# Kernel optimization log

Hardware: AMD Instinct MI355X
Metric: run time of the kernel (lower is better)

The kernel has to match this reference:

```python
import jax, jax.numpy as jnp
import numpy as np

# Config (mirrors HymbaLayer init + env constants)
DIM = 1024; NH = 16; NKV = 4; D = 64          # head_dim = DIM // NH
NATTN = NH // 2; NSSM = NH // 2; KVREP = NATTN // NKV
S = 16          # _HYMBA_SSM_STATE
NMETA = 4       # _HYMBA_META_TOK
BASE = 10000.0  # rope_base
CHUNK = 64      # _HYMBA_SCAN_CHUNK
B, T = 2, 2048


def _rms_norm(x, eps=1e-6):
    return x * jax.lax.rsqrt(jnp.mean(x * x, -1, keepdims=True) + eps)


def _rotary_cs(t_len, d, base):
    inv = 1.0 / (base ** (jnp.arange(0, d, 2, dtype=jnp.float32) / d))  # (d/2,)
    f = jnp.arange(t_len, dtype=jnp.float32)[:, None] * inv[None, :]    # (T, d/2)
    return jnp.cos(f), jnp.sin(f)


def _apply_rot(x, cos, sin):
    # x: (B, H, T, D); rotate-half style rotary
    d2 = x.shape[-1] // 2
    x1, x2 = x[..., :d2], x[..., d2:]
    c, s = cos[None, None], sin[None, None]
    return jnp.concatenate([x1 * c - x2 * s, x1 * s + x2 * c], -1)


def _scan_chunks(log_a, u, chunk):
    # Exact chunk-parallel diagonal scan: h_t = exp(log_a_t)*h_{t-1} + u_t
    b, t, s = u.shape
    nc = t // chunk
    la = log_a.reshape(b, nc, chunk, s)
    uu = u.reshape(b, nc, chunk, s)
    log_p = jnp.clip(jnp.cumsum(la, axis=2), -30.0, 0.0)
    p = jnp.exp(log_p)
    h_local = p * jnp.cumsum(uu * jnp.exp(-log_p), axis=2)

    def step(h0, args):
        hl, pc = args                          # (B, chunk, S)
        hc = hl + pc * h0[:, None, :]
        return hc[:, -1], hc

    _, hs = jax.lax.scan(step, jnp.zeros((b, s), u.dtype),
                         (jnp.swapaxes(h_local, 0, 1), jnp.swapaxes(p, 0, 1)))
    return jnp.swapaxes(hs, 0, 1).reshape(b, t, s)


def _mamba_head(logA, Bw, Cw, dtw, dtb, Ow, x):
    # x: (B, T, D); selective SSM with diagonal A
    dt = jnp.minimum(jax.nn.softplus(x @ dtw.T + dtb), 1.0)   # (B,T,S)
    A = jnp.minimum(-jnp.exp(logA), 10.0)                      # (S,)
    log_a = jnp.clip(dt * A, -0.5, 0.0)
    Bx = (x @ Bw.T) * dt
    Cc = x @ Cw.T
    h = _scan_chunks(log_a, Bx, CHUNK)                         # (B,T,S)
    y = jnp.sum(Cc * h, -1, keepdims=True)
    return h @ Ow.T + y * x[..., :1]


def _forward(x, meta_tokens, c_q_w, c_k_w, c_v_w, q_gain, ssm_in_w, proj_w,
             attn_scale, ssm_scale, ssm_logA, ssm_Bw, ssm_Cw, ssm_dtw, ssm_dtb, ssm_Ow):
    b, t, c = x.shape
    x_ext = jnp.concatenate([jnp.broadcast_to(meta_tokens, (b, NMETA, c)), x], 1)
    t_ext = t + NMETA
    q = (x_ext @ c_q_w.T).reshape(b, t_ext, NH, D).transpose(0, 2, 1, 3)
    k = (x_ext @ c_k_w.T).reshape(b, t_ext, NKV, D).transpose(0, 2, 1, 3)
    v = (x_ext @ c_v_w.T).reshape(b, t_ext, NKV, D).transpose(0, 2, 1, 3)
    q = _rms_norm(q); k = _rms_norm(k)
    cos, sin = _rotary_cs(t_ext, D, BASE)
    q = _apply_rot(q, cos, sin); k = _apply_rot(k, cos, sin)
    # GQA attention over the first NATTN heads, causal over T_ext
    q_attn = q[:, :NATTN] * q_gain[None, :, None, None]
    k_exp = jnp.repeat(k, KVREP, axis=1)
    v_exp = jnp.repeat(v, KVREP, axis=1)
    scores = jnp.einsum('bhqd,bhkd->bhqk', q_attn, k_exp) / jnp.sqrt(jnp.float32(D))
    mask = jnp.tril(jnp.ones((t_ext, t_ext), bool))
    scores = jnp.where(mask[None, None], scores, -jnp.inf)
    attn = jax.nn.softmax(scores, axis=-1)
    ao = jnp.einsum('bhqk,bhkd->bhqd', attn, v_exp)
    ao = ao[:, :, NMETA:].transpose(0, 2, 1, 3).reshape(b, t, NATTN * D) * attn_scale
    # SSM branch on the original (un-prepended) tokens
    ssm_x = (x @ ssm_in_w.T).reshape(b, t, NSSM, D)
    ssm_out = jax.vmap(_mamba_head, in_axes=(0, 0, 0, 0, 0, 0, 2), out_axes=2)(
        ssm_logA, ssm_Bw, ssm_Cw, ssm_dtw, ssm_dtb, ssm_Ow, ssm_x)
    ssm_out = ssm_out.reshape(b, t, NSSM * D) * ssm_scale
    return jnp.concatenate([ao, ssm_out], -1) @ proj_w.T


def setup_inputs() -> dict:
    key = jax.random.key(0)
    ks = jax.random.split(key, 16)
    r = lambda k, sh, sc=0.02: jax.random.normal(k, sh, jnp.float32) * sc
    return {
        'x': jax.random.normal(ks[0], (B, T, DIM), jnp.float32),
        'meta_tokens': r(ks[1], (1, NMETA, DIM)),
        'c_q_w': r(ks[2], (DIM, DIM)),
        'c_k_w': r(ks[3], (NKV * D, DIM)),
        'c_v_w': r(ks[4], (NKV * D, DIM)),
        'q_gain': jnp.full((NATTN,), 1.0, jnp.float32),
        'ssm_in_w': r(ks[5], (NSSM * D, DIM)),
        'proj_w': r(ks[6], (DIM, DIM)),
        'attn_scale': jnp.ones((1,), jnp.float32),
        'ssm_scale': jnp.ones((1,), jnp.float32),
        'ssm_logA': jax.random.normal(ks[7], (NSSM, S), jnp.float32) * 0.5,
        'ssm_Bw': r(ks[8], (NSSM, S, D), 0.05),
        'ssm_Cw': r(ks[9], (NSSM, S, D), 0.05),
        'ssm_dtw': r(ks[10], (NSSM, S, D), 0.05),
        'ssm_dtb': jnp.full((NSSM, S), -4.0, jnp.float32),
        'ssm_Ow': r(ks[11], (NSSM, D, S), 0.05),
    }


def reference(x, meta_tokens, c_q_w, c_k_w, c_v_w, q_gain, ssm_in_w, proj_w,
              attn_scale, ssm_scale, ssm_logA, ssm_Bw, ssm_Cw, ssm_dtw, ssm_dtb, ssm_Ow):
    return _forward(x, meta_tokens, c_q_w, c_k_w, c_v_w, q_gain, ssm_in_w, proj_w,
                    attn_scale, ssm_scale, ssm_logA, ssm_Bw, ssm_Cw, ssm_dtw, ssm_dtb, ssm_Ow)
```

## Files before the change

kernel.cpp:

```cpp
#include <hip/hip_runtime.h>
#include <hip/hip_bf16.h>
#include <math.h>

typedef __hip_bfloat16 bf16;
typedef __attribute__((ext_vector_type(8))) short short8;
typedef __attribute__((ext_vector_type(4))) float f32x4;

static constexpr int kB = 2;
static constexpr int kT = 2048;
static constexpr int kDIM = 1024;
static constexpr int kNMETA = 4;
static constexpr int kTEXT = kT + kNMETA;
static constexpr int kMEXT = kB * kTEXT;
static constexpr int kMPAD = 4224;
static constexpr int kMX = kB * kT;
static constexpr int kQT = 33;
static constexpr int kTP = 2112;

static constexpr size_t oXE = 0;
static constexpr size_t oYB = 0;
static constexpr size_t oLU = 8650752;
static constexpr size_t oCC = oLU + (size_t)kMX * 128 * 8;
static constexpr size_t oHL = oCC + (size_t)kMX * 128 * 4;
static constexpr size_t oPB = oHL + (size_t)kMX * 128 * 2;
static constexpr size_t oCH = oPB + (size_t)kMX * 128 * 2;
static constexpr size_t oCP = oCH + 16384 * 4;
static constexpr size_t oH0 = oCP + 16384 * 4;
static constexpr size_t oSX = oLU + (size_t)kMX * 128 * 8 + (size_t)kMX * 128 * 12;
static constexpr size_t oQP = oSX + (size_t)kMX * 512 * 2;
static constexpr size_t oKP = oQP + (size_t)kB * 8 * kTP * 64 * 2;
static constexpr size_t oVT = oKP + (size_t)kB * 4 * kTP * 64 * 2;
static constexpr size_t oWP = oVT + (size_t)kB * 4 * 64 * kTP * 2;
static constexpr size_t oWQ = oWP + (size_t)1024 * 1024 * 2;
static constexpr size_t oAO = 100663296;
static constexpr size_t oAL = oAO + (size_t)2 * kB * 8 * kTP * 64 * 4;

#define GLD_LDS16(gp, lp)                                                          \
  __builtin_amdgcn_global_load_lds((const __attribute__((address_space(1))) void*)(gp), \
                                   (__attribute__((address_space(3))) void*)(lp), 16, 0, 0)

__device__ __forceinline__ uint4 pack8(float4 a, float4 b) {
  union { bf16 h[8]; uint4 v; } u;
  u.h[0] = __float2bfloat16(a.x); u.h[1] = __float2bfloat16(a.y);
  u.h[2] = __float2bfloat16(a.z); u.h[3] = __float2bfloat16(a.w);
  u.h[4] = __float2bfloat16(b.x); u.h[5] = __float2bfloat16(b.y);
  u.h[6] = __float2bfloat16(b.z); u.h[7] = __float2bfloat16(b.w);
  return u.v;
}

__global__ __launch_bounds__(256) void prep_all(const float* __restrict__ cq, const float* __restrict__ ck,
                                                const float* __restrict__ cv, const float* __restrict__ sw,
                                                const float* __restrict__ pw,
                                                const float* __restrict__ x, const float* __restrict__ meta,
                                                bf16* __restrict__ wqkvsx, bf16* __restrict__ wproj,
                                                bf16* __restrict__ xe,
                                                bf16* __restrict__ Qp, bf16* __restrict__ Kp,
                                                bf16* __restrict__ Vt) {
  int i = blockIdx.x * 256 + threadIdx.x;
  if (i < 327680) {
    int row = i >> 7, v = i & 127;
    const float* src; bf16* dst;
    if (row < 512)       { src = cq + (size_t)row * 1024;          dst = wqkvsx + (size_t)row * 1024; }
    else if (row < 768)  { src = ck + (size_t)(row - 512) * 1024;  dst = wqkvsx + (size_t)row * 1024; }
    else if (row < 1024) { src = cv + (size_t)(row - 768) * 1024;  dst = wqkvsx + (size_t)row * 1024; }
    else if (row < 1536) { src = sw + (size_t)(row - 1024) * 1024; dst = wqkvsx + (size_t)row * 1024; }
    else                 { src = pw + (size_t)(row - 1536) * 1024; dst = wproj + (size_t)(row - 1536) * 1024; }
    float4 a0 = ((const float4*)src)[v * 2], a1 = ((const float4*)src)[v * 2 + 1];
    ((uint4*)dst)[v] = pack8(a0, a1);
  } else if (i < 868352) {
    int j = i - 327680;
    int r = j >> 7, v = j & 127;
    uint4 val = {0u, 0u, 0u, 0u};
    if (r < kMEXT) {
      int b = r / kTEXT, te = r - b * kTEXT;
      const float* src = (te < kNMETA) ? (meta + (size_t)te * kDIM)
                                       : (x + ((size_t)b * kT + (te - kNMETA)) * kDIM);
      float4 a0 = ((const float4*)src)[v * 2];
      float4 a1 = ((const float4*)src)[v * 2 + 1];
      val = pack8(a0, a1);
    }
    ((uint4*)(xe + (size_t)r * kDIM))[v] = val;
  } else {
    int j = i - 868352;
    if (j < 30720) {
      int k = j & 31, te = (j >> 5) % 60, bh = j / (60 * 32);
      *(unsigned int*)(Qp + ((size_t)bh * kTP + 2052 + te) * 64 + k * 2) = 0u;
    } else if (j < 46080) {
      int jj = j - 30720;
      int k = jj & 31, te = (jj >> 5) % 60, bh = jj / (60 * 32);
      *(unsigned int*)(Kp + ((size_t)bh * kTP + 2052 + te) * 64 + k * 2) = 0u;
    } else if (j < 61440) {
      int jj = j - 46080;
      int k = jj % 30, rowd = jj / 30;
      *(unsigned int*)(Vt + (size_t)rowd * kTP + 2052 + k * 2) = 0u;
    }
  }
}

template <int MODE>
__global__ __launch_bounds__(256) void gemm_t(const bf16* __restrict__ A,
                                              const bf16* __restrict__ W,
                                              void* __restrict__ O0, void* __restrict__ O1,
                                              void* __restrict__ O2, void* __restrict__ O3,
                                              const float* __restrict__ q_gain) {
  __shared__ short As[128 * 32];
  __shared__ short Bs[64 * 32];
  const int tid = threadIdx.x;
  const int wave = tid >> 6, lane = tid & 63;
  const int quad = lane >> 4, l16 = lane & 15;
  const int bm = blockIdx.y * 128, bn = blockIdx.x * 64;
  const int srow = tid >> 2, scol = (tid & 3) * 8;
  const bf16* ag0 = A + (size_t)(bm + srow) * 1024 + scol;
  const bf16* ag1 = A + (size_t)(bm + 64 + srow) * 1024 + scol;
  const bf16* bg0 = W + (size_t)(bn + srow) * 1024 + scol;
  char* asb = (char*)As + wave * 1024;
  char* bsb = (char*)Bs + wave * 1024;
  f32x4 acc[2][4] = {};
  for (int k0 = 0; k0 < 1024; k0 += 32) {
    __syncthreads();
    GLD_LDS16(ag0, asb);
    GLD_LDS16(ag1, asb + 4096);
    GLD_LDS16(bg0, bsb);
    ag0 += 32; ag1 += 32; bg0 += 32;
    __syncthreads();
    short8 af[2], bfr[4];
#pragma unroll
    for (int mi = 0; mi < 2; ++mi)
      af[mi] = *(const short8*)((const char*)As + (size_t)(wave * 32 + mi * 16 + l16) * 64 + quad * 16);
#pragma unroll
    for (int ni = 0; ni < 4; ++ni)
      bfr[ni] = *(const short8*)((const char*)Bs + (size_t)(ni * 16 + l16) * 64 + quad * 16);
#pragma unroll
    for (int mi = 0; mi < 2; ++mi)
#pragma unroll
      for (int ni = 0; ni < 4; ++ni)
        acc[mi][ni] = __builtin_amdgcn_mfma_f32_16x16x32_bf16(af[mi], bfr[ni], acc[mi][ni], 0, 0, 0);
  }
  if constexpr (MODE == 2) {
#pragma unroll
    for (int mi = 0; mi < 2; ++mi)
#pragma unroll
      for (int ni = 0; ni < 4; ++ni) {
        int colg = bn + ni * 16 + l16;
#pragma unroll
        for (int r = 0; r < 4; ++r) {
          int row = bm + wave * 32 + mi * 16 + quad * 4 + r;
          ((float*)O0)[(size_t)row * 1024 + colg] = acc[mi][ni][r];
        }
      }
  } else {
    const int tile = blockIdx.x;
    if (tile < 16) {
      float gain = (tile < 8) ? q_gain[tile] * 0.125f : 1.f;
      float inv0 = exp2f(-13.287712379549449f * (float)l16 * (1.f / 32.f));
      float inv1 = exp2f(-13.287712379549449f * (float)(l16 + 16) * (1.f / 32.f));
#pragma unroll
      for (int mi = 0; mi < 2; ++mi) {
        int row0 = bm + wave * 32 + mi * 16 + quad * 4;
        if (row0 >= kMEXT) continue;
        int b = row0 >= kTEXT ? 1 : 0;
        int te0 = row0 - b * kTEXT;
        if (tile < 12) {
          float ss[4];
#pragma unroll
          for (int r = 0; r < 4; ++r) {
            float s = 0.f;
#pragma unroll
            for (int ni = 0; ni < 4; ++ni) s += acc[mi][ni][r] * acc[mi][ni][r];
#pragma unroll
            for (int off = 1; off < 16; off <<= 1) s += __shfl_xor(s, off, 64);
            ss[r] = s;
          }
          bf16* base = (tile < 8)
            ? (bf16*)O0 + (((size_t)(b * 8 + tile)) * kTP + te0) * 64 + l16
            : (bf16*)O1 + (((size_t)(b * 4 + tile - 8)) * kTP + te0) * 64 + l16;
#pragma unroll
          for (int r = 0; r < 4; ++r) {
            float rn = rsqrtf(ss[r] * (1.f / 64.f) + 1e-6f) * gain;
            float te = (float)(te0 + r);
            float a0 = te * inv0, a1 = te * inv1;
            float c0 = __cosf(a0), s0 = __sinf(a0);
            float c1 = __cosf(a1), s1 = __sinf(a1);
            float v0 = acc[mi][0][r] * rn, v1 = acc[mi][1][r] * rn;
            float v2 = acc[mi][2][r] * rn, v3 = acc[mi][3][r] * rn;
            bf16* dst = base + (size_t)r * 64;
            dst[0]  = __float2bfloat16(v0 * c0 - v2 * s0);
            dst[16] = __float2bfloat16(v1 * c1 - v3 * s1);
            dst[32] = __float2bfloat16(v0 * s0 + v2 * c0);
            dst[48] = __float2bfloat16(v1 * s1 + v3 * c1);
          }
        } else {
          int hv = tile - 12;
#pragma unroll
          for (int ni = 0; ni < 4; ++ni) {
            union { unsigned long long q; bf16 hh[4]; } pw;
#pragma unroll
            for (int r = 0; r < 4; ++r) pw.hh[r] = __float2bfloat16(acc[mi][ni][r]);
            *(unsigned long long*)((bf16*)O2 +
                (((size_t)(b * 4 + hv)) * 64 + ni * 16 + l16) * kTP + te0) = pw.q;
          }
        }
      }
    } else {
#pragma unroll
      for (int mi = 0; mi < 2; ++mi)
#pragma unroll
        for (int ni = 0; ni < 4; ++ni) {
          int colg = bn - 1024 + ni * 16 + l16;
#pragma unroll
          for (int r = 0; r < 4; ++r) {
            int row = bm + wave * 32 + mi * 16 + quad * 4 + r;
            if (row < kMEXT) {
              int bb = row >= kTEXT ? 1 : 0;
              int te = row - bb * kTEXT;
              if (te >= kNMETA)
                ((bf16*)O3)[((size_t)(bb * kT + te - kNMETA)) * 512 + colg] =
                    __float2bfloat16(acc[mi][ni][r]);
            }
          }
        }
    }
  }
}

__global__ __launch_bounds__(256) void attn_part(const bf16* __restrict__ Qp,
                                                 const bf16* __restrict__ Kp,
                                                 const bf16* __restrict__ Vt,
                                                 float* __restrict__ AO, float* __restrict__ AL) {
  __shared__ short Ks[64][72];
  __shared__ short Vs[64][72];
  __shared__ short Ps[4][16][72];
  const int part = blockIdx.x & 1;
  const int qt = (kQT - 1) - (blockIdx.x >> 1);
  const int h = blockIdx.y, b = blockIdx.z;
  const int kvh = h >> 1;
  const int tid = threadIdx.x, wave = tid >> 6, lane = tid & 63;
  const int quad = lane >> 4, l16 = lane & 15;
  const int hsplit = (qt + 2) >> 1;
  const int kt_begin = part == 0 ? 0 : hsplit;
  const int kt_end = part == 0 ? hsplit : qt + 1;

  short8 qf[2];
  {
    const bf16* qrow = Qp + (((size_t)(b * 8 + h)) * kTP + qt * 64 + wave * 16 + l16) * 64 + quad * 8;
    qf[0] = *(const short8*)(qrow);
    qf[1] = *(const short8*)(qrow + 32);
  }
  short8 ones;
#pragma unroll
  for (int i = 0; i < 8; ++i) ones[i] = (short)0x3F80;

  const bf16* kbase = Kp + ((size_t)(b * 4 + kvh)) * kTP * 64;
  const bf16* vbase = Vt + ((size_t)(b * 4 + kvh)) * 64 * kTP;

  const int r0row = tid >> 3, r0c8 = tid & 7;
  const int r1row = (256 + tid) >> 3, r1c8 = tid & 7;

  f32x4 O[4] = {};
  f32x4 lacc = {};
  const int q_abs = qt * 64 + wave * 16 + l16;

  uint4 kr0 = *(const uint4*)(kbase + (size_t)(kt_begin * 64 + r0row) * 64 + r0c8 * 8);
  uint4 kr1 = *(const uint4*)(kbase + (size_t)(kt_begin * 64 + r1row) * 64 + r1c8 * 8);
  uint4 vr0 = *(const uint4*)(vbase + (size_t)r0row * kTP + kt_begin * 64 + r0c8 * 8);
  uint4 vr1 = *(const uint4*)(vbase + (size_t)r1row * kTP + kt_begin * 64 + r1c8 * 8);

  for (int kt = kt_begin; kt < kt_end; ++kt) {
    __syncthreads();
    *(uint4*)&Ks[r0row][r0c8 * 8] = kr0;
    *(uint4*)&Ks[r1row][r1c8 * 8] = kr1;
    *(uint4*)&Vs[r0row][r0c8 * 8] = vr0;
    *(uint4*)&Vs[r1row][r1c8 * 8] = vr1;
    if (kt + 1 < kt_end) {
      int kn = (kt + 1) * 64;
      kr0 = *(const uint4*)(kbase + (size_t)(kn + r0row) * 64 + r0c8 * 8);
      kr1 = *(const uint4*)(kbase + (size_t)(kn + r1row) * 64 + r1c8 * 8);
      vr0 = *(const uint4*)(vbase + (size_t)r0row * kTP + kn + r0c8 * 8);
      vr1 = *(const uint4*)(vbase + (size_t)r1row * kTP + kn + r1c8 * 8);
    }
    __syncthreads();

    f32x4 st[4] = {};
#pragma unroll
    for (int nb = 0; nb < 4; ++nb) {
      short8 ak0 = *(const short8*)&Ks[nb * 16 + l16][quad * 8];
      st[nb] = __builtin_amdgcn_mfma_f32_16x16x32_bf16(ak0, qf[0], st[nb], 0, 0, 0);
      short8 ak1 = *(const short8*)&Ks[nb * 16 + l16][32 + quad * 8];
      st[nb] = __builtin_amdgcn_mfma_f32_16x16x32_bf16(ak1, qf[1], st[nb], 0, 0, 0);
    }
    if (kt == qt) {
      int key0 = kt * 64 + quad * 4;
#pragma unroll
      for (int nb = 0; nb < 4; ++nb)
#pragma unroll
        for (int rg = 0; rg < 4; ++rg)
          if (key0 + nb * 16 + rg > q_abs) st[nb][rg] = -1e30f;
    }
#pragma unroll
    for (int nb = 0; nb < 4; ++nb) {
      union { unsigned long long q; bf16 hh[4]; } pw;
#pragma unroll
      for (int rg = 0; rg < 4; ++rg) pw.hh[rg] = __float2bfloat16(__expf(st[nb][rg]));
      *(unsigned long long*)&Ps[wave][l16][nb * 16 + quad * 4] = pw.q;
    }
    short8 pf0 = *(const short8*)&Ps[wave][l16][quad * 8];
    short8 pf1 = *(const short8*)&Ps[wave][l16][32 + quad * 8];
    lacc = __builtin_amdgcn_mfma_f32_16x16x32_bf16(pf0, ones, lacc, 0, 0, 0);
    lacc = __builtin_amdgcn_mfma_f32_16x16x32_bf16(pf1, ones, lacc, 0, 0, 0);
#pragma unroll
    for (int db = 0; db < 4; ++db) {
      short8 bv0 = *(const short8*)&Vs[db * 16 + l16][quad * 8];
      O[db] = __builtin_amdgcn_mfma_f32_16x16x32_bf16(pf0, bv0, O[db], 0, 0, 0);
      short8 bv1 = *(const short8*)&Vs[db * 16 + l16][32 + quad * 8];
      O[db] = __builtin_amdgcn_mfma_f32_16x16x32_bf16(pf1, bv1, O[db], 0, 0, 0);
    }
  }
  size_t hb = (((size_t)part * 2 + b) * 8 + h);
  float* aoB = AO + hb * kTP * 64;
  float* alB = AL + hb * kTP;
#pragma unroll
  for (int rg = 0; rg < 4; ++rg) {
    int q = qt * 64 + wave * 16 + quad * 4 + rg;
    float* dst = aoB + (size_t)q * 64 + l16;
#pragma unroll
    for (int db = 0; db < 4; ++db) dst[db * 16] = O[db][rg];
    if (l16 == 0) alB[q] = lacc[rg];
  }
}

__global__ __launch_bounds__(256) void ssm_prep(const bf16* __restrict__ sx,
                                                const float* __restrict__ dtw, const float* __restrict__ dtb,
                                                const float* __restrict__ Bw, const float* __restrict__ Cw,
                                                const float* __restrict__ logA,
                                                float* __restrict__ LU, float* __restrict__ Cc) {
  __shared__ short Xs[64][72];
  __shared__ short Ws[48][72];
  const int bm = blockIdx.x * 64, h = blockIdx.y;
  const int tid = threadIdx.x, wave = tid >> 6, lane = tid & 63;
  const int quad = lane >> 4, l16 = lane & 15;
#pragma unroll
  for (int is = 0; is < 2; ++is) {
    int e = is * 256 + tid;
    int row = e >> 3, v = e & 7;
    uint4 val = *(const uint4*)(sx + ((size_t)(bm + row)) * 512 + h * 64 + v * 8);
    *(uint4*)&Xs[row][v * 8] = val;
  }
#pragma unroll
  for (int is = 0; is < 2; ++is) {
    int s = is * 256 + tid;
    if (s < 384) {
      int row = s >> 3, v = s & 7;
      const float* src = (row < 16) ? dtw + ((size_t)(h * 16 + row)) * 64
                       : (row < 32) ? Bw + ((size_t)(h * 16 + row - 16)) * 64
                                    : Cw + ((size_t)(h * 16 + row - 32)) * 64;
      float4 a0 = ((const float4*)src)[v * 2];
      float4 a1 = ((const float4*)src)[v * 2 + 1];
      *(uint4*)&Ws[row][v * 8] = pack8(a0, a1);
    }
  }
  __syncthreads();
  short8 af0 = *(const short8*)&Xs[wave * 16 + l16][quad * 8];
  short8 af1 = *(const short8*)&Xs[wave * 16 + l16][32 + quad * 8];
  f32x4 acc[3] = {};
#pragma unroll
  for (int nb = 0; nb < 3; ++nb) {
    short8 b0 = *(const short8*)&Ws[nb * 16 + l16][quad * 8];
    acc[nb] = __builtin_amdgcn_mfma_f32_16x16x32_bf16(af0, b0, acc[nb], 0, 0, 0);
    short8 b1 = *(const short8*)&Ws[nb * 16 + l16][32 + quad * 8];
    acc[nb] = __builtin_amdgcn_mfma_f32_16x16x32_bf16(af1, b1, acc[nb], 0, 0, 0);
  }
  float dtb_v = dtb[h * 16 + l16];
  float A_v = fminf(-expf(logA[h * 16 + l16]), 10.f);
#pragma unroll
  for (int rg = 0; rg < 4; ++rg) {
    int bt = bm + wave * 16 + quad * 4 + rg;
    size_t ix = (size_t)bt * 128 + h * 16 + l16;
    float raw = acc[0][rg] + dtb_v;
    float sp = fmaxf(raw, 0.f) + log1pf(expf(-fabsf(raw)));
    float dt = fminf(sp, 1.f);
    float lav = fminf(fmaxf(dt * A_v, -0.5f), 0.f);
    *(float2*)(LU + 2 * ix) = make_float2(lav, acc[1][rg] * dt);
    Cc[ix] = acc[2][rg];
  }
}

__global__ __launch_bounds__(256) void ssm_scan1(const float* __restrict__ LU,
                                                 bf16* __restrict__ hloc, bf16* __restrict__ Pb,
                                                 float* __restrict__ chHt, float* __restrict__ chPt) {
  int id = blockIdx.x * 256 + threadIdx.x;
  if (id >= 16384) return;
  int hs = id & 127, c = (id >> 7) & 63, b = id >> 13;
  float hv = 0.f, cum = 0.f;
  size_t base = ((size_t)b * kT) * 128 + hs;
  const float2* LU2 = (const float2*)LU;
  for (int i = 0; i < 32; ++i) {
    size_t ix = base + (size_t)(c * 32 + i) * 128;
    float2 lu = LU2[ix];
    cum += lu.x;
    hv = expf(lu.x) * hv + lu.y;
    hloc[ix] = __float2bfloat16(hv);
    Pb[ix] = __float2bfloat16(expf(fmaxf(cum, -30.f)));
  }
  int t = b * 8192 + hs * 64 + c;
  chHt[t] = hv;
  chPt[t] = expf(fmaxf(cum, -30.f));
}

__global__ __launch_bounds__(256) void ssm_scan2(const float* __restrict__ chHt,
                                                 const float* __restrict__ chPt,
                                                 float* __restrict__ h0) {
  int id = blockIdx.x * 256 + threadIdx.x;
  int c = id & 63;
  int chain = id >> 6;
  int b = chain >> 7, hs = chain & 127;
  int t = b * 8192 + hs * 64 + c;
  float H = chHt[t], P = chPt[t];
#pragma unroll
  for (int off = 1; off < 64; off <<= 1) {
    float Hp = __shfl_up(H, off, 64);
    float Pp = __shfl_up(P, off, 64);
    if (c >= off) { H = H + P * Hp; P = P * Pp; }
  }
  float Hex = __shfl_up(H, 1, 64);
  if (c == 0) Hex = 0.f;
  h0[b * 8192 + c * 128 + hs] = Hex;
}

__global__ __launch_bounds__(256) void combine_out(const float* __restrict__ AO,
                                                   const float* __restrict__ AL,
                                                   const float* __restrict__ attn_scale,
                                                   const bf16* __restrict__ hloc, const bf16* __restrict__ Pb,
                                                   const float* __restrict__ h0, const float* __restrict__ Cc,
                                                   const bf16* __restrict__ sx, const float* __restrict__ Ow,
                                                   const float* __restrict__ ssm_scale,
                                                   bf16* __restrict__ Y) {
  if (blockIdx.x < 528) {
    int id = blockIdx.x * 256 + threadIdx.x;
    int d16 = id & 3;
    int tmp = id >> 2;
    int q = tmp % kTP; tmp /= kTP;
    int h = tmp & 7, b = tmp >> 3;
    if (q < kNMETA || q >= kTEXT) return;
    size_t hb0 = ((size_t)b * 8 + h), hb1 = ((size_t)(2 + b) * 8 + h);
    float l = AL[hb0 * kTP + q] + AL[hb1 * kTP + q];
    float so = attn_scale[0] / fmaxf(l, 1e-30f);
    const float4* p0 = (const float4*)(AO + (hb0 * kTP + q) * 64 + d16 * 16);
    const float4* p1 = (const float4*)(AO + (hb1 * kTP + q) * 64 + d16 * 16);
    bf16* dst = Y + ((size_t)(b * kT + q - kNMETA)) * kDIM + h * 64 + d16 * 16;
#pragma unroll
    for (int i = 0; i < 4; ++i) {
      float4 a = p0[i], c = p1[i];
      dst[i * 4 + 0] = __float2bfloat16((a.x + c.x) * so);
      dst[i * 4 + 1] = __float2bfloat16((a.y + c.y) * so);
      dst[i * 4 + 2] = __float2bfloat16((a.z + c.z) * so);
      dst[i * 4 + 3] = __float2bfloat16((a.w + c.w) * so);
    }
  } else {
    int id = (blockIdx.x - 528) * 256 + threadIdx.x;
    int d4 = id & 3, h = (id >> 2) & 7, t = (id >> 5) & 2047, b = id >> 16;
    size_t ix0 = ((size_t)(b * kT + t)) * 128 + h * 16;
    int h0b = b * 8192 + (t >> 5) * 128 + h * 16;
    float hv[16], y = 0.f;
#pragma unroll
    for (int s = 0; s < 16; ++s) {
      float v = __bfloat162float(hloc[ix0 + s]) + __bfloat162float(Pb[ix0 + s]) * h0[h0b + s];
      hv[s] = v;
      y += Cc[ix0 + s] * v;
    }
    float x0 = __bfloat162float(sx[((size_t)(b * kT + t)) * 512 + h * 64]);
    float scl = ssm_scale[0];
    const float* ow = Ow + ((size_t)h * 64 + d4 * 16) * 16;
    bf16* dst = Y + ((size_t)(b * kT + t)) * kDIM + 512 + h * 64 + d4 * 16;
    float yx = y * x0;
#pragma unroll
    for (int d = 0; d < 16; ++d) {
      float acc = yx;
      const float* owr = ow + d * 16;
#pragma unroll
      for (int s = 0; s < 16; ++s) acc += hv[s] * owr[s];
      dst[d] = __float2bfloat16(acc * scl);
    }
  }
}

extern "C" void kernel_launch(void* const* d_in, const int* in_sizes, int n_in,
                              void* d_out, int out_size, void* d_ws, size_t ws_size,
                              hipStream_t stream) {
  (void)in_sizes; (void)n_in; (void)out_size; (void)ws_size;
  const float* x        = (const float*)d_in[0];
  const float* meta     = (const float*)d_in[1];
  const float* c_q_w    = (const float*)d_in[2];
  const float* c_k_w    = (const float*)d_in[3];
  const float* c_v_w    = (const float*)d_in[4];
  const float* q_gain   = (const float*)d_in[5];
  const float* ssm_in_w = (const float*)d_in[6];
  const float* proj_w   = (const float*)d_in[7];
  const float* attn_sc  = (const float*)d_in[8];
  const float* ssm_sc   = (const float*)d_in[9];
  const float* ssm_logA = (const float*)d_in[10];
  const float* ssm_Bw   = (const float*)d_in[11];
  const float* ssm_Cw   = (const float*)d_in[12];
  const float* ssm_dtw  = (const float*)d_in[13];
  const float* ssm_dtb  = (const float*)d_in[14];
  const float* ssm_Ow   = (const float*)d_in[15];

  char* w = (char*)d_ws;
  bf16*  XE = (bf16*)(w + oXE);
  bf16*  SX = (bf16*)(w + oSX);
  bf16*  YB = (bf16*)(w + oYB);
  bf16*  QP = (bf16*)(w + oQP);
  bf16*  KP = (bf16*)(w + oKP);
  bf16*  VT = (bf16*)(w + oVT);
  bf16*  WQ = (bf16*)(w + oWQ);
  bf16*  WP = (bf16*)(w + oWP);
  float* LU = (float*)(w + oLU);
  float* CC = (float*)(w + oCC);
  bf16*  HL = (bf16*)(w + oHL);
  bf16*  PB = (bf16*)(w + oPB);
  float* CH = (float*)(w + oCH);
  float* CP = (float*)(w + oCP);
  float* H0 = (float*)(w + oH0);
  float* AO = (float*)(w + oAO);
  float* AL = (float*)(w + oAL);

  prep_all<<<3632, 256, 0, stream>>>(c_q_w, c_k_w, c_v_w, ssm_in_w, proj_w,
                                     x, meta, WQ, WP, XE, QP, KP, VT);

  gemm_t<0><<<dim3(24, kMPAD / 128), 256, 0, stream>>>(XE, WQ, QP, KP, VT, SX, q_gain);

  attn_part<<<dim3(kQT * 2, 8, kB), 256, 0, stream>>>(QP, KP, VT, AO, AL);

  ssm_prep<<<dim3(kMX / 64, 8), 256, 0, stream>>>(SX, ssm_dtw, ssm_dtb, ssm_Bw, ssm_Cw,
                                                  ssm_logA, LU, CC);
  ssm_scan1<<<64, 256, 0, stream>>>(LU, HL, PB, CH, CP);
  ssm_scan2<<<64, 256, 0, stream>>>(CH, CP, H0);

  combine_out<<<1040, 256, 0, stream>>>(AO, AL, attn_sc, HL, PB, H0, CC, SX, ssm_Ow, ssm_sc, YB);

  gemm_t<2><<<dim3(16, kMX / 128), 256, 0, stream>>>(YB, WP, d_out, nullptr, nullptr, nullptr, nullptr);
}
```

Baseline: 215.7 us.

## Fuse SSM input projection into QKV GEMM epilogue and merge scan passes

The SSM dt/B/C projection moves into the epilogue of the QKV GEMM, which works on the SSM-input tile from registers and LDS. This removes the separate ssm_prep kernel and the bf16 SX intermediate; only x0 per head is kept for combine_out. The two scan kernels become one kernel that computes chunk totals, scans across chunks in a wave, and then rescans to write the final h directly, dropping the Pb and h0 buffers. In exchange the scan reads LU twice, the GEMM epilogue does more work and uses more shared memory, and the final h is now computed in a sequential rescan rather than from bf16 partials.

```diff
diff --git a/kernel.cpp b/kernel.cpp
--- a/kernel.cpp
+++ b/kernel.cpp
@@ -22,22 +22,24 @@
 static constexpr size_t oLU = 8650752;
 static constexpr size_t oCC = oLU + (size_t)kMX * 128 * 8;
 static constexpr size_t oHL = oCC + (size_t)kMX * 128 * 4;
-static constexpr size_t oPB = oHL + (size_t)kMX * 128 * 2;
-static constexpr size_t oCH = oPB + (size_t)kMX * 128 * 2;
-static constexpr size_t oCP = oCH + 16384 * 4;
-static constexpr size_t oH0 = oCP + 16384 * 4;
-static constexpr size_t oSX = oLU + (size_t)kMX * 128 * 8 + (size_t)kMX * 128 * 12;
-static constexpr size_t oQP = oSX + (size_t)kMX * 512 * 2;
+static constexpr size_t oX0 = oHL + (size_t)kMX * 128 * 2;
+static constexpr size_t oQP = oX0 + (size_t)kMX * 8 * 4;
 static constexpr size_t oKP = oQP + (size_t)kB * 8 * kTP * 64 * 2;
 static constexpr size_t oVT = oKP + (size_t)kB * 4 * kTP * 64 * 2;
 static constexpr size_t oWP = oVT + (size_t)kB * 4 * 64 * kTP * 2;
 static constexpr size_t oWQ = oWP + (size_t)1024 * 1024 * 2;
-static constexpr size_t oAO = 100663296;
+static constexpr size_t oAO = 134217728;
 static constexpr size_t oAL = oAO + (size_t)2 * kB * 8 * kTP * 64 * 4;
 
 #define GLD_LDS16(gp, lp)                                                          \
   __builtin_amdgcn_global_load_lds((const __attribute__((address_space(1))) void*)(gp), \
                                    (__attribute__((address_space(3))) void*)(lp), 16, 0, 0)
+
+__device__ __forceinline__ short bf2s(float f) {
+  union { bf16 h; short s; } u;
+  u.h = __float2bfloat16(f);
+  return u.s;
+}
 
 __device__ __forceinline__ uint4 pack8(float4 a, float4 b) {
   union { bf16 h[8]; uint4 v; } u;
@@ -101,10 +103,15 @@
 __global__ __launch_bounds__(256) void gemm_t(const bf16* __restrict__ A,
                                               const bf16* __restrict__ W,
                                               void* __restrict__ O0, void* __restrict__ O1,
-                                              void* __restrict__ O2, void* __restrict__ O3,
-                                              const float* __restrict__ q_gain) {
-  __shared__ short As[128 * 32];
-  __shared__ short Bs[64 * 32];
+                                              void* __restrict__ O2,
+                                              const float* __restrict__ q_gain,
+                                              const float* __restrict__ dtw, const float* __restrict__ dtb,
+                                              const float* __restrict__ Bw, const float* __restrict__ Cw,
+                                              const float* __restrict__ logA,
+                                              float* __restrict__ LU, float* __restrict__ CC,
+                                              float* __restrict__ X0) {
+  constexpr int SMEM_SZ = (MODE == 0) ? 25344 : 12288;
+  __shared__ char smem[SMEM_SZ];
   const int tid = threadIdx.x;
   const int wave = tid >> 6, lane = tid & 63;
   const int quad = lane >> 4, l16 = lane & 15;
@@ -113,8 +120,8 @@
   const bf16* ag0 = A + (size_t)(bm + srow) * 1024 + scol;
   const bf16* ag1 = A + (size_t)(bm + 64 + srow) * 1024 + scol;
   const bf16* bg0 = W + (size_t)(bn + srow) * 1024 + scol;
-  char* asb = (char*)As + wave * 1024;
-  char* bsb = (char*)Bs + wave * 1024;
+  char* asb = smem + wave * 1024;
+  char* bsb = smem + 8192 + wave * 1024;
   f32x4 acc[2][4] = {};
   for (int k0 = 0; k0 < 1024; k0 += 32) {
     __syncthreads();
@@ -126,10 +133,10 @@
     short8 af[2], bfr[4];
 #pragma unroll
     for (int mi = 0; mi < 2; ++mi)
-      af[mi] = *(const short8*)((const char*)As + (size_t)(wave * 32 + mi * 16 + l16) * 64 + quad * 16);
+      af[mi] = *(const short8*)(smem + (size_t)(wave * 32 + mi * 16 + l16) * 64 + quad * 16);
 #pragma unroll
     for (int ni = 0; ni < 4; ++ni)
-      bfr[ni] = *(const short8*)((const char*)Bs + (size_t)(ni * 16 + l16) * 64 + quad * 16);
+      bfr[ni] = *(const short8*)(smem + 8192 + (size_t)(ni * 16 + l16) * 64 + quad * 16);
 #pragma unroll
     for (int mi = 0; mi < 2; ++mi)
 #pragma unroll
@@ -202,22 +209,72 @@
         }
       }
     } else {
-#pragma unroll
-      for (int mi = 0; mi < 2; ++mi)
-#pragma unroll
-        for (int ni = 0; ni < 4; ++ni) {
-          int colg = bn - 1024 + ni * 16 + l16;
+      const int hd = tile - 16;
+      __syncthreads();
+      short (*Xl)[72] = (short(*)[72])smem;
+      short (*Wl)[72] = (short(*)[72])(smem + 18432);
+#pragma unroll
+      for (int mi = 0; mi < 2; ++mi) {
+        if (l16 == 0) {
 #pragma unroll
           for (int r = 0; r < 4; ++r) {
             int row = bm + wave * 32 + mi * 16 + quad * 4 + r;
             if (row < kMEXT) {
               int bb = row >= kTEXT ? 1 : 0;
               int te = row - bb * kTEXT;
-              if (te >= kNMETA)
-                ((bf16*)O3)[((size_t)(bb * kT + te - kNMETA)) * 512 + colg] =
-                    __float2bfloat16(acc[mi][ni][r]);
+              if (te >= kNMETA) X0[(size_t)(bb * kT + te - kNMETA) * 8 + hd] = acc[mi][0][r];
             }
           }
+        }
+      }
+#pragma unroll
+      for (int mi = 0; mi < 2; ++mi)
+#pragma unroll
+        for (int ni = 0; ni < 4; ++ni)
+#pragma unroll
+          for (int r = 0; r < 4; ++r)
+            Xl[wave * 32 + mi * 16 + quad * 4 + r][ni * 16 + l16] = bf2s(acc[mi][ni][r]);
+      for (int s2 = tid; s2 < 384; s2 += 256) {
+        int row = s2 >> 3, v = s2 & 7;
+        const float* src = (row < 16) ? dtw + ((size_t)(hd * 16 + row)) * 64
+                         : (row < 32) ? Bw + ((size_t)(hd * 16 + row - 16)) * 64
+                                      : Cw + ((size_t)(hd * 16 + row - 32)) * 64;
+        float4 a0 = ((const float4*)src)[v * 2];
+        float4 a1 = ((const float4*)src)[v * 2 + 1];
+        *(uint4*)&Wl[row][v * 8] = pack8(a0, a1);
+      }
+      __syncthreads();
+      f32x4 a3[2][3] = {};
+#pragma unroll
+      for (int mt = 0; mt < 2; ++mt) {
+        short8 xa0 = *(const short8*)&Xl[wave * 32 + mt * 16 + l16][quad * 8];
+        short8 xa1 = *(const short8*)&Xl[wave * 32 + mt * 16 + l16][32 + quad * 8];
+#pragma unroll
+        for (int nb = 0; nb < 3; ++nb) {
+          short8 wb0 = *(const short8*)&Wl[nb * 16 + l16][quad * 8];
+          a3[mt][nb] = __builtin_amdgcn_mfma_f32_16x16x32_bf16(xa0, wb0, a3[mt][nb], 0, 0, 0);
+          short8 wb1 = *(const short8*)&Wl[nb * 16 + l16][32 + quad * 8];
+          a3[mt][nb] = __builtin_amdgcn_mfma_f32_16x16x32_bf16(xa1, wb1, a3[mt][nb], 0, 0, 0);
+        }
+      }
+      float dtb_v = dtb[hd * 16 + l16];
+      float A_v = fminf(-expf(logA[hd * 16 + l16]), 10.f);
+#pragma unroll
+      for (int mt = 0; mt < 2; ++mt)
+#pragma unroll
+        for (int r = 0; r < 4; ++r) {
+          int row = bm + wave * 32 + mt * 16 + quad * 4 + r;
+          if (row >= kMEXT) continue;
+          int bb = row >= kTEXT ? 1 : 0;
+          int te = row - bb * kTEXT;
+          if (te < kNMETA) continue;
+          size_t ix = (size_t)(bb * kT + te - kNMETA) * 128 + hd * 16 + l16;
+          float raw = a3[mt][0][r] + dtb_v;
+          float sp = fmaxf(raw, 0.f) + log1pf(expf(-fabsf(raw)));
+          float dt = fminf(sp, 1.f);
+          float lav = fminf(fmaxf(dt * A_v, -0.5f), 0.f);
+          *(float2*)(LU + 2 * ix) = make_float2(lav, a3[mt][1][r] * dt);
+          CC[ix] = a3[mt][2][r];
         }
     }
   }
@@ -328,110 +385,49 @@
   }
 }
 
-__global__ __launch_bounds__(256) void ssm_prep(const bf16* __restrict__ sx,
-                                                const float* __restrict__ dtw, const float* __restrict__ dtb,
-                                                const float* __restrict__ Bw, const float* __restrict__ Cw,
-                                                const float* __restrict__ logA,
-                                                float* __restrict__ LU, float* __restrict__ Cc) {
-  __shared__ short Xs[64][72];
-  __shared__ short Ws[48][72];
-  const int bm = blockIdx.x * 64, h = blockIdx.y;
-  const int tid = threadIdx.x, wave = tid >> 6, lane = tid & 63;
-  const int quad = lane >> 4, l16 = lane & 15;
-#pragma unroll
-  for (int is = 0; is < 2; ++is) {
-    int e = is * 256 + tid;
-    int row = e >> 3, v = e & 7;
-    uint4 val = *(const uint4*)(sx + ((size_t)(bm + row)) * 512 + h * 64 + v * 8);
-    *(uint4*)&Xs[row][v * 8] = val;
-  }
-#pragma unroll
-  for (int is = 0; is < 2; ++is) {
-    int s = is * 256 + tid;
-    if (s < 384) {
-      int row = s >> 3, v = s & 7;
-      const float* src = (row < 16) ? dtw + ((size_t)(h * 16 + row)) * 64
-                       : (row < 32) ? Bw + ((size_t)(h * 16 + row - 16)) * 64
-                                    : Cw + ((size_t)(h * 16 + row - 32)) * 64;
-      float4 a0 = ((const float4*)src)[v * 2];
-      float4 a1 = ((const float4*)src)[v * 2 + 1];
-      *(uint4*)&Ws[row][v * 8] = pack8(a0, a1);
-    }
-  }
+__global__ __launch_bounds__(256) void ssm_scan(const float* __restrict__ LU, bf16* __restrict__ HL) {
+  __shared__ float sH[4][64], sP[4][64], sH0[4][64];
+  const int tid = threadIdx.x;
+  const int ch = tid & 3, c = tid >> 2;
+  const int chain = blockIdx.x * 4 + ch;
+  const int b = chain >> 7, hs = chain & 127;
+  const float2* LU2 = (const float2*)LU;
+  const size_t base = ((size_t)b * kT) * 128 + hs;
+  float H = 0.f, cum = 0.f;
+  for (int i = 0; i < 32; ++i) {
+    float2 lu = LU2[base + (size_t)(c * 32 + i) * 128];
+    cum += lu.x;
+    H = __expf(lu.x) * H + lu.y;
+  }
+  sH[ch][c] = H;
+  sP[ch][c] = __expf(cum);
   __syncthreads();
-  short8 af0 = *(const short8*)&Xs[wave * 16 + l16][quad * 8];
-  short8 af1 = *(const short8*)&Xs[wave * 16 + l16][32 + quad * 8];
-  f32x4 acc[3] = {};
-#pragma unroll
-  for (int nb = 0; nb < 3; ++nb) {
-    short8 b0 = *(const short8*)&Ws[nb * 16 + l16][quad * 8];
-    acc[nb] = __builtin_amdgcn_mfma_f32_16x16x32_bf16(af0, b0, acc[nb], 0, 0, 0);
-    short8 b1 = *(const short8*)&Ws[nb * 16 + l16][32 + quad * 8];
-    acc[nb] = __builtin_amdgcn_mfma_f32_16x16x32_bf16(af1, b1, acc[nb], 0, 0, 0);
-  }
-  float dtb_v = dtb[h * 16 + l16];
-  float A_v = fminf(-expf(logA[h * 16 + l16]), 10.f);
-#pragma unroll
-  for (int rg = 0; rg < 4; ++rg) {
-    int bt = bm + wave * 16 + quad * 4 + rg;
-    size_t ix = (size_t)bt * 128 + h * 16 + l16;
-    float raw = acc[0][rg] + dtb_v;
-    float sp = fmaxf(raw, 0.f) + log1pf(expf(-fabsf(raw)));
-    float dt = fminf(sp, 1.f);
-    float lav = fminf(fmaxf(dt * A_v, -0.5f), 0.f);
-    *(float2*)(LU + 2 * ix) = make_float2(lav, acc[1][rg] * dt);
-    Cc[ix] = acc[2][rg];
-  }
-}
-
-__global__ __launch_bounds__(256) void ssm_scan1(const float* __restrict__ LU,
-                                                 bf16* __restrict__ hloc, bf16* __restrict__ Pb,
-                                                 float* __restrict__ chHt, float* __restrict__ chPt) {
-  int id = blockIdx.x * 256 + threadIdx.x;
-  if (id >= 16384) return;
-  int hs = id & 127, c = (id >> 7) & 63, b = id >> 13;
-  float hv = 0.f, cum = 0.f;
-  size_t base = ((size_t)b * kT) * 128 + hs;
-  const float2* LU2 = (const float2*)LU;
+  const int wv = tid >> 6, lane = tid & 63;
+  float Hs = sH[wv][lane], Ps = sP[wv][lane];
+#pragma unroll
+  for (int off = 1; off < 64; off <<= 1) {
+    float Hp = __shfl_up(Hs, off, 64);
+    float Pp = __shfl_up(Ps, off, 64);
+    if (lane >= off) { Hs = Hs + Ps * Hp; Ps = Ps * Pp; }
+  }
+  float Hex = __shfl_up(Hs, 1, 64);
+  if (lane == 0) Hex = 0.f;
+  sH0[wv][lane] = Hex;
+  __syncthreads();
+  float h = sH0[ch][c];
   for (int i = 0; i < 32; ++i) {
     size_t ix = base + (size_t)(c * 32 + i) * 128;
     float2 lu = LU2[ix];
-    cum += lu.x;
-    hv = expf(lu.x) * hv + lu.y;
-    hloc[ix] = __float2bfloat16(hv);
-    Pb[ix] = __float2bfloat16(expf(fmaxf(cum, -30.f)));
-  }
-  int t = b * 8192 + hs * 64 + c;
-  chHt[t] = hv;
-  chPt[t] = expf(fmaxf(cum, -30.f));
-}
-
-__global__ __launch_bounds__(256) void ssm_scan2(const float* __restrict__ chHt,
-                                                 const float* __restrict__ chPt,
-                                                 float* __restrict__ h0) {
-  int id = blockIdx.x * 256 + threadIdx.x;
-  int c = id & 63;
-  int chain = id >> 6;
-  int b = chain >> 7, hs = chain & 127;
-  int t = b * 8192 + hs * 64 + c;
-  float H = chHt[t], P = chPt[t];
-#pragma unroll
-  for (int off = 1; off < 64; off <<= 1) {
-    float Hp = __shfl_up(H, off, 64);
-    float Pp = __shfl_up(P, off, 64);
-    if (c >= off) { H = H + P * Hp; P = P * Pp; }
-  }
-  float Hex = __shfl_up(H, 1, 64);
-  if (c == 0) Hex = 0.f;
-  h0[b * 8192 + c * 128 + hs] = Hex;
+    h = __expf(lu.x) * h + lu.y;
+    HL[ix] = __float2bfloat16(h);
+  }
 }
 
 __global__ __launch_bounds__(256) void combine_out(const float* __restrict__ AO,
                                                    const float* __restrict__ AL,
                                                    const float* __restrict__ attn_scale,
-                                                   const bf16* __restrict__ hloc, const bf16* __restrict__ Pb,
-                                                   const float* __restrict__ h0, const float* __restrict__ Cc,
-                                                   const bf16* __restrict__ sx, const float* __restrict__ Ow,
+                                                   const bf16* __restrict__ HL, const float* __restrict__ CC,
+                                                   const float* __restrict__ X0, const float* __restrict__ Ow,
                                                    const float* __restrict__ ssm_scale,
                                                    bf16* __restrict__ Y) {
   if (blockIdx.x < 528) {
@@ -459,15 +455,14 @@
     int id = (blockIdx.x - 528) * 256 + threadIdx.x;
     int d4 = id & 3, h = (id >> 2) & 7, t = (id >> 5) & 2047, b = id >> 16;
     size_t ix0 = ((size_t)(b * kT + t)) * 128 + h * 16;
-    int h0b = b * 8192 + (t >> 5) * 128 + h * 16;
     float hv[16], y = 0.f;
 #pragma unroll
     for (int s = 0; s < 16; ++s) {
-      float v = __bfloat162float(hloc[ix0 + s]) + __bfloat162float(Pb[ix0 + s]) * h0[h0b + s];
+      float v = __bfloat162float(HL[ix0 + s]);
       hv[s] = v;
-      y += Cc[ix0 + s] * v;
-    }
-    float x0 = __bfloat162float(sx[((size_t)(b * kT + t)) * 512 + h * 64]);
+      y += CC[ix0 + s] * v;
+    }
+    float x0 = X0[(size_t)(b * kT + t) * 8 + h];
     float scl = ssm_scale[0];
     const float* ow = Ow + ((size_t)h * 64 + d4 * 16) * 16;
     bf16* dst = Y + ((size_t)(b * kT + t)) * kDIM + 512 + h * 64 + d4 * 16;
@@ -506,7 +501,6 @@
 
   char* w = (char*)d_ws;
   bf16*  XE = (bf16*)(w + oXE);
-  bf16*  SX = (bf16*)(w + oSX);
   bf16*  YB = (bf16*)(w + oYB);
   bf16*  QP = (bf16*)(w + oQP);
   bf16*  KP = (bf16*)(w + oKP);
@@ -516,26 +510,24 @@
   float* LU = (float*)(w + oLU);
   float* CC = (float*)(w + oCC);
   bf16*  HL = (bf16*)(w + oHL);
-  bf16*  PB = (bf16*)(w + oPB);
-  float* CH = (float*)(w + oCH);
-  float* CP = (float*)(w + oCP);
-  float* H0 = (float*)(w + oH0);
+  float* X0 = (float*)(w + oX0);
   float* AO = (float*)(w + oAO);
   float* AL = (float*)(w + oAL);
 
   prep_all<<<3632, 256, 0, stream>>>(c_q_w, c_k_w, c_v_w, ssm_in_w, proj_w,
                                      x, meta, WQ, WP, XE, QP, KP, VT);
 
-  gemm_t<0><<<dim3(24, kMPAD / 128), 256, 0, stream>>>(XE, WQ, QP, KP, VT, SX, q_gain);
+  gemm_t<0><<<dim3(24, kMPAD / 128), 256, 0, stream>>>(XE, WQ, QP, KP, VT, q_gain,
+                                                       ssm_dtw, ssm_dtb, ssm_Bw, ssm_Cw,
+                                                       ssm_logA, LU, CC, X0);
 
   attn_part<<<dim3(kQT * 2, 8, kB), 256, 0, stream>>>(QP, KP, VT, AO, AL);
 
-  ssm_prep<<<dim3(kMX / 64, 8), 256, 0, stream>>>(SX, ssm_dtw, ssm_dtb, ssm_Bw, ssm_Cw,
-                                                  ssm_logA, LU, CC);
-  ssm_scan1<<<64, 256, 0, stream>>>(LU, HL, PB, CH, CP);
-  ssm_scan2<<<64, 256, 0, stream>>>(CH, CP, H0);
-
-  combine_out<<<1040, 256, 0, stream>>>(AO, AL, attn_sc, HL, PB, H0, CC, SX, ssm_Ow, ssm_sc, YB);
-
-  gemm_t<2><<<dim3(16, kMX / 128), 256, 0, stream>>>(YB, WP, d_out, nullptr, nullptr, nullptr, nullptr);
-}
+  ssm_scan<<<64, 256, 0, stream>>>(LU, HL);
+
+  combine_out<<<1040, 256, 0, stream>>>(AO, AL, attn_sc, HL, CC, X0, ssm_Ow, ssm_sc, YB);
+
+  gemm_t<2><<<dim3(16, kMX / 128), 256, 0, stream>>>(YB, WP, d_out, nullptr, nullptr, nullptr,
+                                                     nullptr, nullptr, nullptr, nullptr, nullptr,
+                                                     nullptr, nullptr, nullptr);
+}
```

New measurement: 226.9 us. 1.05x slower.
